# Kernel tuning notes

Measured on AMD Instinct MI355X. Metric: run time of the kernel, lower is better.

## Reference

```python
import jax, jax.numpy as jnp
import numpy as np

DIM = 2048; H = 16; DK = 128; DV = 128; SEQ = 2048; KCONV = 4
KEY_DIM = H * DK; VAL_DIM = H * DV
EPS_L2 = 1e-6; EPS_RMS = 1e-6; SP_THRESH = 20.0


def setup_inputs() -> dict:
    key = jax.random.key(0)
    ks = jax.random.split(key, 20)
    f = jnp.float32
    def w(k, shape, scale):
        return jax.random.normal(k, shape, f) * scale
    s_in = DIM ** -0.5
    return {
        "x": jax.random.normal(ks[0], (1, SEQ, DIM), f),
        "ve": jax.random.normal(ks[1], (1, SEQ, H, DV), f),
        "sa_lambdas": jnp.array([0.7, 0.3], f),
        "Wq": w(ks[2], (DIM, KEY_DIM), s_in),
        "Wk": w(ks[3], (DIM, KEY_DIM), s_in),
        "Wv": w(ks[4], (DIM, VAL_DIM), s_in),
        "conv_q": w(ks[5], (KEY_DIM, KCONV), 0.5),
        "conv_k": w(ks[6], (KEY_DIM, KCONV), 0.5),
        "conv_v": w(ks[7], (VAL_DIM, KCONV), 0.5),
        "Wf1": w(ks[8], (DIM, DV), s_in),
        "Wf2": w(ks[9], (DV, KEY_DIM), DV ** -0.5),
        "Wb": w(ks[10], (DIM, H), s_in),
        "A_log": jnp.log(jax.random.uniform(ks[11], (H,), f, 1.0, 16.0)),
        "dt_bias": jnp.zeros((KEY_DIM,), f),
        "Wg1": w(ks[12], (DIM, DV), s_in),
        "Wg2": w(ks[13], (DV, VAL_DIM), DV ** -0.5),
        "bg2": jnp.zeros((VAL_DIM,), f),
        "norm_w": jnp.ones((DV,), f),
        "Wo": w(ks[14], (VAL_DIM, DIM), VAL_DIM ** -0.5),
    }


def _short_conv_silu(u, w):
    # u: [b, s, c], w: [c, K]; causal depthwise conv + silu
    s = u.shape[1]
    up = jnp.pad(u, ((0, 0), (w.shape[1] - 1, 0), (0, 0)))
    y = sum(up[:, i:i + s, :] * w[:, i] for i in range(w.shape[1]))
    return jax.nn.silu(y)


def _l2norm(t):
    return t * jax.lax.rsqrt(jnp.sum(t * t, axis=-1, keepdims=True) + EPS_L2)


def _forward(x, ve, sa_lambdas, Wq, Wk, Wv, conv_q, conv_k, conv_v,
             Wf1, Wf2, Wb, A_log, dt_bias, Wg1, Wg2, bg2, norm_w, Wo):
    b, s, _ = x.shape  # b == 1
    q = _short_conv_silu(x @ Wq, conv_q).reshape(b, s, H, DK)
    k = _short_conv_silu(x @ Wk, conv_k).reshape(b, s, H, DK)
    v = _short_conv_silu(x @ Wv, conv_v).reshape(b, s, H, DV)
    v = sa_lambdas[0] * v + sa_lambdas[1] * ve
    # KDA gate: per-(head, key-dim) log decay
    g = ((x @ Wf1) @ Wf2).reshape(b, s, H, DK) + dt_bias.reshape(H, DK)
    sp = jnp.where(g > SP_THRESH, g, jnp.log1p(jnp.exp(jnp.minimum(g, SP_THRESH))))
    glog = -jnp.exp(A_log)[None, None, :, None] * sp  # [b,s,h,dk]
    beta = jax.nn.sigmoid(x @ Wb)  # [b,s,h]
    # l2-normalize q,k; scale q by dk^-0.5 (chunk_kda default scale)
    qn = _l2norm(q) * (DK ** -0.5)
    kn = _l2norm(k)
    # gated delta-rule recurrence over time (b==1, squeeze batch)
    def step(S, inp):
        qt, kt, vt, gt, bt = inp  # [h,dk],[h,dk],[h,dv],[h,dk],[h]
        S = S * jnp.exp(gt)[..., None]  # per-key-channel decay
        pred = jnp.einsum('hk,hkv->hv', kt, S)
        vt_new = bt[:, None] * (vt - pred)
        S = S + kt[:, :, None] * vt_new[:, None, :]
        ot = jnp.einsum('hk,hkv->hv', qt, S)
        return S, ot
    S0 = jnp.zeros((H, DK, DV), x.dtype)
    _, o = jax.lax.scan(step, S0, (qn[0], kn[0], v[0], glog[0], beta[0]))
    o = o[None]  # [1,s,h,dv]
    # sigmoid-gated RMSNorm over head_v_dim
    gate = ((x @ Wg1) @ Wg2 + bg2).reshape(b, s, H, DV)
    var = jnp.mean(o * o, axis=-1, keepdims=True)
    o = o * jax.lax.rsqrt(var + EPS_RMS) * norm_w
    o = o * jax.nn.sigmoid(gate)
    return o.reshape(b, s, VAL_DIM) @ Wo  # [1,s,dim]


def reference(x, ve, sa_lambdas, Wq, Wk, Wv, conv_q, conv_k, conv_v,
              Wf1, Wf2, Wb, A_log, dt_bias, Wg1, Wg2, bg2, norm_w, Wo):
    return _forward(x, ve, sa_lambdas, Wq, Wk, Wv, conv_q, conv_k, conv_v,
                    Wf1, Wf2, Wb, A_log, dt_bias, Wg1, Wg2, bg2, norm_w, Wo)
```

## Files before the change

### kernel.cpp

```cpp
#include <hip/hip_runtime.h>
#include <hip/hip_bf16.h>
#include <stdint.h>
#include <stddef.h>

#define SEQL 2048
#define DIMSZ 2048
#define HN 16
#define DKD 128
#define DVD 128
#define QSCALE 0.08838834764831843f

typedef __attribute__((ext_vector_type(4))) float f32x4;
typedef __attribute__((ext_vector_type(2))) float f32x2;
typedef __attribute__((ext_vector_type(8))) short bf16x8;

__device__ __forceinline__ float sigmoid_f(float x) { return 1.f / (1.f + __expf(-x)); }
__device__ __forceinline__ float bf2f(short s) {
  union { float f; unsigned int u; } t; t.u = ((unsigned int)(unsigned short)s) << 16; return t.f;
}

#define BM 128
#define BN 128
#define BKK 64

__global__ __launch_bounds__(256) void gemm_bt(
    const __hip_bfloat16* __restrict__ A, const __hip_bfloat16* __restrict__ B,
    float* __restrict__ C, int M, int N, int lda, int ldb, int klen, int accum)
{
  __shared__ __hip_bfloat16 As[BM * BKK];
  __shared__ __hip_bfloat16 Bs[BN * BKK];
  const int tid = threadIdx.x;
  const int lane = tid & 63;
  const int w = tid >> 6;
  const int wm = w >> 1, wn = w & 1;
  const int m0 = blockIdx.y * BM, n0 = blockIdx.x * BN;
  const int l15 = lane & 15, l4 = lane >> 4;
  const int kbase = blockIdx.z * klen;

  f32x4 acc[4][4] = {};

  for (int k0 = kbase; k0 < kbase + klen; k0 += BKK) {
#pragma unroll
    for (int i = 0; i < 4; ++i) {
      const int c = (w * 4 + i) * 64 + lane;
      const int row = c >> 3;
      const int colb = (c & 7) * 8;
      __builtin_amdgcn_global_load_lds(
          (const __attribute__((address_space(1))) void*)(A + (size_t)(m0 + row) * lda + k0 + colb),
          (__attribute__((address_space(3))) void*)(As + (size_t)c * 8), 16, 0, 0);
      __builtin_amdgcn_global_load_lds(
          (const __attribute__((address_space(1))) void*)(B + (size_t)(n0 + row) * ldb + k0 + colb),
          (__attribute__((address_space(3))) void*)(Bs + (size_t)c * 8), 16, 0, 0);
    }
    __syncthreads();
#pragma unroll
    for (int kk = 0; kk < BKK; kk += 32) {
      bf16x8 af[4], bfv[4];
#pragma unroll
      for (int mi = 0; mi < 4; ++mi)
        af[mi] = *(const bf16x8*)(As + (wm * 64 + mi * 16 + l15) * BKK + kk + l4 * 8);
#pragma unroll
      for (int ni = 0; ni < 4; ++ni)
        bfv[ni] = *(const bf16x8*)(Bs + (wn * 64 + ni * 16 + l15) * BKK + kk + l4 * 8);
#pragma unroll
      for (int mi = 0; mi < 4; ++mi)
#pragma unroll
        for (int ni = 0; ni < 4; ++ni)
          acc[mi][ni] = __builtin_amdgcn_mfma_f32_16x16x32_bf16(af[mi], bfv[ni], acc[mi][ni], 0, 0, 0);
    }
    __syncthreads();
  }

  float* Cz = C + (size_t)blockIdx.z * M * N;
#pragma unroll
  for (int mi = 0; mi < 4; ++mi) {
#pragma unroll
    for (int ni = 0; ni < 4; ++ni) {
      const int row = m0 + wm * 64 + mi * 16 + l4 * 4;
      const int col = n0 + wn * 64 + ni * 16 + l15;
#pragma unroll
      for (int r = 0; r < 4; ++r) {
        size_t idx = (size_t)(row + r) * N + col;
        if (accum) Cz[idx] += acc[mi][ni][r];
        else Cz[idx] = acc[mi][ni][r];
      }
    }
  }
}

__global__ __launch_bounds__(512, 1) void gemm_bt192(
    const __hip_bfloat16* __restrict__ A, const __hip_bfloat16* __restrict__ B,
    __hip_bfloat16* __restrict__ Cb, int N, int lda, int ldb, int NT)
{
  __shared__ __hip_bfloat16 lds[57344];
  const int tid = threadIdx.x;
  const int w = tid >> 6, lane = tid & 63;
  const int wm = w >> 2, wn = w & 3;
  const int l15 = lane & 15, l4 = lane >> 4;
  const int m0 = blockIdx.y * 256, n0 = blockIdx.x * 192;

  f32x4 acc[8][3] = {};
  bf16x8 a[4][2], b[2];

  auto stage_a = [&](int half, int t1) {
    const int buf = t1 & 1;
    const int k0n = ((t1 < NT) ? t1 : 0) * 64;
#pragma unroll
    for (int i = 0; i < 2; ++i) {
      const int c = i * 512 + tid;
      const int l = half * 128 + (c >> 3);
      const int kcs = (c & 7) ^ (l & 7);
      const int grow = ((l >> 6) & 1) * 128 + (l >> 7) * 64 + (l & 63);
      __builtin_amdgcn_global_load_lds(
          (const __attribute__((address_space(1))) void*)(A + (size_t)(m0 + grow) * lda + k0n + kcs * 8),
          (__attribute__((address_space(3))) void*)(lds + (size_t)buf * 28672 + half * 8192 + (size_t)c * 8),
          16, 0, 0);
    }
  };
  auto stage_b = [&](int j, int t1) {
    const int buf = t1 & 1;
    const int k0n = ((t1 < NT) ? t1 : 0) * 64;
    const int c = tid;
    const int l = j * 64 + (c >> 3);
    const int kcs = (c & 7) ^ (l & 7);
    __builtin_amdgcn_global_load_lds(
        (const __attribute__((address_space(1))) void*)(B + (size_t)(n0 + l) * ldb + k0n + kcs * 8),
        (__attribute__((address_space(3))) void*)(lds + (size_t)buf * 28672 + 16384 + j * 4096 + (size_t)c * 8),
        16, 0, 0);
  };

  auto phase = [&](size_t cb, int MQ, int NQ, bool needA) {
    if (needA) {
#pragma unroll
      for (int m2 = 0; m2 < 4; ++m2)
#pragma unroll
        for (int ks = 0; ks < 2; ++ks) {
          const int la = MQ * 128 + wm * 64 + m2 * 16 + l15;
          const int kc = ks * 4 + l4;
          a[m2][ks] = *(const bf16x8*)(lds + cb + la * 64 + (kc ^ (la & 7)) * 8);
        }
    }
#pragma unroll
    for (int ks = 0; ks < 2; ++ks) {
      const int lb = NQ * 64 + wn * 16 + l15;
      const int kc = ks * 4 + l4;
      b[ks] = *(const bf16x8*)(lds + cb + 16384 + lb * 64 + (kc ^ (lb & 7)) * 8);
    }
    __builtin_amdgcn_s_setprio(1);
#pragma unroll
    for (int m2 = 0; m2 < 4; ++m2)
#pragma unroll
      for (int ks = 0; ks < 2; ++ks)
        acc[MQ * 4 + m2][NQ] = __builtin_amdgcn_mfma_f32_16x16x32_bf16(
            a[m2][ks], b[ks], acc[MQ * 4 + m2][NQ], 0, 0, 0);
    __builtin_amdgcn_s_setprio(0);
  };

  stage_a(0, 0); stage_a(1, 0); stage_b(0, 0); stage_b(1, 0); stage_b(2, 0);

  for (int t = 0; t < NT; ++t) {
    const size_t cb = (size_t)(t & 1) * 28672;
    stage_a(0, t + 1);
    asm volatile("s_waitcnt vmcnt(4)" ::: "memory");
    __builtin_amdgcn_s_barrier();
    __builtin_amdgcn_sched_barrier(0);
    phase(cb, 0, 0, true);
    __builtin_amdgcn_s_barrier();
    stage_a(1, t + 1);
    asm volatile("s_waitcnt vmcnt(5)" ::: "memory");
    __builtin_amdgcn_s_barrier();
    __builtin_amdgcn_sched_barrier(0);
    phase(cb, 0, 1, false);
    __builtin_amdgcn_s_barrier();
    stage_b(0, t + 1);
    asm volatile("s_waitcnt vmcnt(5)" ::: "memory");
    __builtin_amdgcn_s_barrier();
    __builtin_amdgcn_sched_barrier(0);
    phase(cb, 0, 2, false);
    __builtin_amdgcn_s_barrier();
    stage_b(1, t + 1);
    __builtin_amdgcn_s_barrier();
    __builtin_amdgcn_sched_barrier(0);
    phase(cb, 1, 0, true);
    __builtin_amdgcn_s_barrier();
    stage_b(2, t + 1);
    __builtin_amdgcn_s_barrier();
    __builtin_amdgcn_sched_barrier(0);
    phase(cb, 1, 1, false);
    __builtin_amdgcn_s_barrier();
    __builtin_amdgcn_s_barrier();
    __builtin_amdgcn_sched_barrier(0);
    phase(cb, 1, 2, false);
    __builtin_amdgcn_s_barrier();
  }
  asm volatile("s_waitcnt vmcnt(0)" ::: "memory");

#pragma unroll
  for (int mi = 0; mi < 8; ++mi)
#pragma unroll
    for (int nq = 0; nq < 3; ++nq) {
      const int row = m0 + wm * 128 + mi * 16 + l4 * 4;
      const int col = n0 + nq * 64 + wn * 16 + l15;
#pragma unroll
      for (int r = 0; r < 4; ++r)
        Cb[(size_t)(row + r) * N + col] = __float2bfloat16(acc[mi][nq][r]);
    }
}

__global__ __launch_bounds__(256) void gemm_btsplit(
    const __hip_bfloat16* __restrict__ Ah, const __hip_bfloat16* __restrict__ Al,
    const __hip_bfloat16* __restrict__ Bh, const __hip_bfloat16* __restrict__ Bl,
    float* __restrict__ C, int M, int N, int lda, int ldb, int klen)
{
  __shared__ __hip_bfloat16 Ash[BM * BKK];
  __shared__ __hip_bfloat16 Asl[BM * BKK];
  __shared__ __hip_bfloat16 Bsh[BN * BKK];
  __shared__ __hip_bfloat16 Bsl[BN * BKK];
  const int tid = threadIdx.x;
  const int lane = tid & 63;
  const int w = tid >> 6;
  const int wm = w >> 1, wn = w & 1;
  const int m0 = blockIdx.y * BM, n0 = blockIdx.x * BN;
  const int l15 = lane & 15, l4 = lane >> 4;
  const int kbase = blockIdx.z * klen;

  f32x4 acc[4][4] = {};

  for (int k0 = kbase; k0 < kbase + klen; k0 += BKK) {
#pragma unroll
    for (int i = 0; i < 4; ++i) {
      const int c = (w * 4 + i) * 64 + lane;
      const int row = c >> 3;
      const int colb = (c & 7) * 8;
      const size_t go = (size_t)(m0 + row) * lda + k0 + colb;
      const size_t gn = (size_t)(n0 + row) * ldb + k0 + colb;
      __builtin_amdgcn_global_load_lds(
          (const __attribute__((address_space(1))) void*)(Ah + go),
          (__attribute__((address_space(3))) void*)(Ash + (size_t)c * 8), 16, 0, 0);
      __builtin_amdgcn_global_load_lds(
          (const __attribute__((address_space(1))) void*)(Al + go),
          (__attribute__((address_space(3))) void*)(Asl + (size_t)c * 8), 16, 0, 0);
      __builtin_amdgcn_global_load_lds(
          (const __attribute__((address_space(1))) void*)(Bh + gn),
          (__attribute__((address_space(3))) void*)(Bsh + (size_t)c * 8), 16, 0, 0);
      __builtin_amdgcn_global_load_lds(
          (const __attribute__((address_space(1))) void*)(Bl + gn),
          (__attribute__((address_space(3))) void*)(Bsl + (size_t)c * 8), 16, 0, 0);
    }
    __syncthreads();
#pragma unroll
    for (int kk = 0; kk < BKK; kk += 32) {
      bf16x8 afh[4], afl[4], bfh[4], bfl[4];
#pragma unroll
      for (int mi = 0; mi < 4; ++mi) {
        const int ao = (wm * 64 + mi * 16 + l15) * BKK + kk + l4 * 8;
        afh[mi] = *(const bf16x8*)(Ash + ao);
        afl[mi] = *(const bf16x8*)(Asl + ao);
      }
#pragma unroll
      for (int ni = 0; ni < 4; ++ni) {
        const int bo = (wn * 64 + ni * 16 + l15) * BKK + kk + l4 * 8;
        bfh[ni] = *(const bf16x8*)(Bsh + bo);
        bfl[ni] = *(const bf16x8*)(Bsl + bo);
      }
#pragma unroll
      for (int mi = 0; mi < 4; ++mi)
#pragma unroll
        for (int ni = 0; ni < 4; ++ni) {
          acc[mi][ni] = __builtin_amdgcn_mfma_f32_16x16x32_bf16(afh[mi], bfh[ni], acc[mi][ni], 0, 0, 0);
          acc[mi][ni] = __builtin_amdgcn_mfma_f32_16x16x32_bf16(afh[mi], bfl[ni], acc[mi][ni], 0, 0, 0);
          acc[mi][ni] = __builtin_amdgcn_mfma_f32_16x16x32_bf16(afl[mi], bfh[ni], acc[mi][ni], 0, 0, 0);
        }
    }
    __syncthreads();
  }

  float* Cz = C + (size_t)blockIdx.z * M * N;
#pragma unroll
  for (int mi = 0; mi < 4; ++mi) {
#pragma unroll
    for (int ni = 0; ni < 4; ++ni) {
      const int row = m0 + wm * 64 + mi * 16 + l4 * 4;
      const int col = n0 + wn * 64 + ni * 16 + l15;
#pragma unroll
      for (int r = 0; r < 4; ++r)
        Cz[(size_t)(row + r) * N + col] = acc[mi][ni][r];
    }
  }
}

__global__ __launch_bounds__(256) void prep_all_kernel(
    const float* __restrict__ x, __hip_bfloat16* __restrict__ xb, __hip_bfloat16* __restrict__ xlo,
    const float* __restrict__ Wq, const float* __restrict__ Wk,
    const float* __restrict__ Wv, const float* __restrict__ Wo,
    __hip_bfloat16* __restrict__ WqkvT, __hip_bfloat16* __restrict__ WoT,
    const float* __restrict__ Wf1, const float* __restrict__ Wg1,
    __hip_bfloat16* __restrict__ fg1h, __hip_bfloat16* __restrict__ fg1l,
    const float* __restrict__ Wf2, const float* __restrict__ Wg2,
    __hip_bfloat16* __restrict__ f2h, __hip_bfloat16* __restrict__ f2l,
    __hip_bfloat16* __restrict__ g2h)
{
  __shared__ float tile[32][33];
  const int bid = blockIdx.x;
  const int tid = threadIdx.x;
  const int tc = tid & 31, tr = tid >> 5;

  if (bid < 16384) {
    const int z = bid >> 12, rem = bid & 4095;
    const int c0 = (rem & 63) * 32, r0 = (rem >> 6) * 32;
    const float* in = (z == 0) ? Wq : (z == 1) ? Wk : (z == 2) ? Wv : Wo;
    __hip_bfloat16* outT = (z < 3) ? (WqkvT + (size_t)z * 2048 * 2048) : WoT;
#pragma unroll
    for (int i = 0; i < 4; ++i)
      tile[tr + i * 8][tc] = in[(size_t)(r0 + tr + i * 8) * 2048 + c0 + tc];
    __syncthreads();
#pragma unroll
    for (int i = 0; i < 4; ++i)
      outT[(size_t)(c0 + tr + i * 8) * 2048 + r0 + tc] = __float2bfloat16(tile[tc][tr + i * 8]);
  } else if (bid < 16896) {
    const int rem = bid - 16384;
    const int z = rem >> 8, within = rem & 255;
    const int c0 = (within & 3) * 32, r0 = (within >> 2) * 32;
    const float* in = z ? Wg1 : Wf1;
    const size_t base = (size_t)z * 128 * 2048;
#pragma unroll
    for (int i = 0; i < 4; ++i)
      tile[tr + i * 8][tc] = in[(size_t)(r0 + tr + i * 8) * 128 + c0 + tc];
    __syncthreads();
#pragma unroll
    for (int i = 0; i < 4; ++i) {
      float val = tile[tc][tr + i * 8];
      __hip_bfloat16 h = __float2bfloat16(val);
      size_t oi = base + (size_t)(c0 + tr + i * 8) * 2048 + r0 + tc;
      fg1h[oi] = h;
      fg1l[oi] = z ? __float2bfloat16(0.f) : __float2bfloat16(val - __bfloat162float(h));
    }
  } else if (bid < 17408) {
    const int rem = bid - 16896;
    const int z = rem >> 8, within = rem & 255;
    const int c0 = (within & 63) * 32, r0 = (within >> 6) * 32;
    const float* in = z ? Wg2 : Wf2;
#pragma unroll
    for (int i = 0; i < 4; ++i)
      tile[tr + i * 8][tc] = in[(size_t)(r0 + tr + i * 8) * 2048 + c0 + tc];
    __syncthreads();
#pragma unroll
    for (int i = 0; i < 4; ++i) {
      float val = tile[tc][tr + i * 8];
      __hip_bfloat16 h = __float2bfloat16(val);
      size_t oi = (size_t)(c0 + tr + i * 8) * 128 + r0 + tc;
      if (z == 0) { f2h[oi] = h; f2l[oi] = __float2bfloat16(val - __bfloat162float(h)); }
      else g2h[oi] = h;
    }
  } else {
    const int idx = (bid - 17408) * 256 + tid;
    f32x4 v = *(const f32x4*)(x + (size_t)idx * 4);
    union { __hip_bfloat16 b[4]; unsigned long long u; } ph, pl;
#pragma unroll
    for (int j = 0; j < 4; ++j) {
      float f = v[j];
      __hip_bfloat16 hh = __float2bfloat16(f);
      ph.b[j] = hh;
      pl.b[j] = __float2bfloat16(f - __bfloat162float(hh));
    }
    *(unsigned long long*)((char*)xb + (size_t)idx * 8) = ph.u;
    *(unsigned long long*)((char*)xlo + (size_t)idx * 8) = pl.u;
  }
}

__global__ __launch_bounds__(256) void reduce8_beta_kernel(
    const float* __restrict__ part, __hip_bfloat16* __restrict__ hi,
    __hip_bfloat16* __restrict__ lo, size_t chunk,
    const float* __restrict__ x, const float* __restrict__ Wb, float* __restrict__ betaT)
{
  const int tid = threadIdx.x;
  if (blockIdx.x < 512) {
    int idx = blockIdx.x * 256 + tid;
    f32x4 a = *(const f32x4*)(part + (size_t)idx * 4);
#pragma unroll
    for (int z = 1; z < 8; ++z) {
      f32x4 b = *(const f32x4*)(part + z * chunk + (size_t)idx * 4);
      a.x += b.x; a.y += b.y; a.z += b.z; a.w += b.w;
    }
    union { __hip_bfloat16 b[4]; unsigned long long u; } ph, pl;
#pragma unroll
    for (int j = 0; j < 4; ++j) {
      float f = a[j];
      __hip_bfloat16 hh = __float2bfloat16(f);
      ph.b[j] = hh;
      pl.b[j] = __float2bfloat16(f - __bfloat162float(hh));
    }
    *(unsigned long long*)((char*)hi + (size_t)idx * 8) = ph.u;
    *(unsigned long long*)((char*)lo + (size_t)idx * 8) = pl.u;
  } else {
    int idx = (blockIdx.x - 512) * 256 + tid;
    int s = idx >> 4, h = idx & 15;
    const float* xr = x + (size_t)s * DIMSZ;
    float acc = 0.f;
    for (int d = 0; d < DIMSZ; d += 4) {
      f32x4 xv = *(const f32x4*)(xr + d);
      acc = fmaf(xv.x, Wb[(size_t)(d + 0) * HN + h], acc);
      acc = fmaf(xv.y, Wb[(size_t)(d + 1) * HN + h], acc);
      acc = fmaf(xv.z, Wb[(size_t)(d + 2) * HN + h], acc);
      acc = fmaf(xv.w, Wb[(size_t)(d + 3) * HN + h], acc);
    }
    betaT[(size_t)h * SEQL + s] = 1.f / (1.f + expf(-acc));
  }
}

#define SL20(r, d) ((r) * 160 + ((d) >> 4) * 20 + ((d) & 15))

__global__ __launch_bounds__(256) void kda_pref(
    const __hip_bfloat16* __restrict__ qkv, const float* __restrict__ ve,
    const float* __restrict__ lam,
    const float* __restrict__ cwq, const float* __restrict__ cwk, const float* __restrict__ cwv,
    const float* __restrict__ gbuf,
    const float* __restrict__ dtb, const float* __restrict__ A_log,
    const float* __restrict__ betaT,
    __hip_bfloat16* __restrict__ Xgh, __hip_bfloat16* __restrict__ KTh,
    float* __restrict__ uvS, float* __restrict__ olocS, float* __restrict__ Pg)
{
  __shared__ float GL2[32 * 160];
  __shared__ float kL2[32 * 160];
  __shared__ float qL2[32 * 132];
  __shared__ float vL2[32 * 128];
  __shared__ float ALB[32][33];
  __shared__ float Bdiag[32], betaL[32];
  __shared__ float csumW[4 * 128];

  const int bid = blockIdx.x;
  const int h = bid >> 6, cc = bid & 63;
  const int tid = threadIdx.x;
  const int w = tid >> 6, lane = tid & 63;
  const size_t hc = (size_t)h * 64 + cc;
  const float Aexp = __expf(A_log[h]);

  {
    const int c = lane * 2;
    const int r0g = cc * 32 + w * 8;
    const int cg = h * 128 + c;

    f32x4 wq0 = *(const f32x4*)(cwq + (size_t)cg * 4), wq1 = *(const f32x4*)(cwq + (size_t)(cg + 1) * 4);
    f32x4 wk0 = *(const f32x4*)(cwk + (size_t)cg * 4), wk1 = *(const f32x4*)(cwk + (size_t)(cg + 1) * 4);
    f32x4 wv0 = *(const f32x4*)(cwv + (size_t)cg * 4), wv1 = *(const f32x4*)(cwv + (size_t)(cg + 1) * 4);
    f32x2 dt2 = *(const f32x2*)(dtb + cg);
    const float l0 = lam[0], l1 = lam[1];

    f32x2 xqr[11], xkr[11], xvr[11];
#pragma unroll
    for (int i = 0; i < 11; ++i) {
      const int sr = r0g - 3 + i;
      if (sr >= 0) {
        const size_t ro = (size_t)sr * 6144 + cg;
        unsigned int uq = *(const unsigned int*)(qkv + ro);
        unsigned int uk = *(const unsigned int*)(qkv + 2048 + ro);
        unsigned int uv2 = *(const unsigned int*)(qkv + 4096 + ro);
        xqr[i].x = bf2f((short)uq);   xqr[i].y = bf2f((short)(uq >> 16));
        xkr[i].x = bf2f((short)uk);   xkr[i].y = bf2f((short)(uk >> 16));
        xvr[i].x = bf2f((short)uv2);  xvr[i].y = bf2f((short)(uv2 >> 16));
      } else {
        xqr[i].x = xqr[i].y = xkr[i].x = xkr[i].y = xvr[i].x = xvr[i].y = 0.f;
      }
    }

    float gl0[8], gl1[8];
#pragma unroll
    for (int i = 0; i < 8; ++i) {
      const int rr = r0g + i;
      const int lr = w * 8 + i;
      float aq0 = 0, aq1 = 0, ak0 = 0, ak1 = 0, av0 = 0, av1 = 0;
#pragma unroll
      for (int j = 0; j < 4; ++j) {
        aq0 = fmaf(xqr[i + j].x, wq0[j], aq0); aq1 = fmaf(xqr[i + j].y, wq1[j], aq1);
        ak0 = fmaf(xkr[i + j].x, wk0[j], ak0); ak1 = fmaf(xkr[i + j].y, wk1[j], ak1);
        av0 = fmaf(xvr[i + j].x, wv0[j], av0); av1 = fmaf(xvr[i + j].y, wv1[j], av1);
      }
      float yq0 = aq0 * sigmoid_f(aq0), yq1 = aq1 * sigmoid_f(aq1);
      float yk0 = ak0 * sigmoid_f(ak0), yk1 = ak1 * sigmoid_f(ak1);
      float yv0 = av0 * sigmoid_f(av0), yv1 = av1 * sigmoid_f(av1);

      f32x2 vev = *(const f32x2*)(ve + ((size_t)rr * HN + h) * 128 + c);
      float v0 = l0 * yv0 + l1 * vev.x;
      float v1 = l0 * yv1 + l1 * vev.y;

      float ssq = yq0 * yq0 + yq1 * yq1;
      float ssk = yk0 * yk0 + yk1 * yk1;
#pragma unroll
      for (int off = 32; off > 0; off >>= 1) {
        ssq += __shfl_xor(ssq, off);
        ssk += __shfl_xor(ssk, off);
      }
      float rq = rsqrtf(ssq + 1e-6f) * QSCALE;
      float rk = rsqrtf(ssk + 1e-6f);

      f32x2 kk; kk.x = yk0 * rk; kk.y = yk1 * rk;
      f32x2 qq; qq.x = yq0 * rq; qq.y = yq1 * rq;
      f32x2 vv; vv.x = v0; vv.y = v1;
      *(f32x2*)&kL2[SL20(lr, c)] = kk;
      *(f32x2*)&qL2[lr * 132 + c] = qq;
      *(f32x2*)&vL2[lr * 128 + c] = vv;

      f32x2 gv = *(const f32x2*)(gbuf + (size_t)rr * 2048 + cg);
      float g0 = gv.x + dt2.x, g1 = gv.y + dt2.y;
      float sp0 = (g0 > 20.f) ? g0 : log1pf(__expf(fminf(g0, 20.f)));
      float sp1 = (g1 > 20.f) ? g1 : log1pf(__expf(fminf(g1, 20.f)));
      gl0[i] = -Aexp * sp0;
      gl1[i] = -Aexp * sp1;
    }
    {
      float r0 = 0.f, r1 = 0.f;
#pragma unroll
      for (int i = 0; i < 8; ++i) { r0 += gl0[i]; gl0[i] = r0; r1 += gl1[i]; gl1[i] = r1; }
      csumW[w * 128 + c] = r0;
      csumW[w * 128 + c + 1] = r1;
    }
    if (tid < 32) betaL[tid] = betaT[(size_t)h * SEQL + cc * 32 + tid];
    __syncthreads();
    {
      float p0 = 0.f, p1 = 0.f;
      for (int wp = 0; wp < w; ++wp) { p0 += csumW[wp * 128 + c]; p1 += csumW[wp * 128 + c + 1]; }
#pragma unroll
      for (int i = 0; i < 8; ++i) {
        f32x2 gg; gg.x = gl0[i] + p0; gg.y = gl1[i] + p1;
        *(f32x2*)&GL2[SL20(w * 8 + i, c)] = gg;
      }
    }
  }
  __syncthreads();

  {
    const int tg = lane >> 3, s8 = lane & 7;
    const int tt = w * 8 + tg;
    const int ds = s8 * 20;

    float Gt[16], kt[16], qt[16];
#pragma unroll
    for (int j = 0; j < 16; j += 4) {
      *(f32x4*)&Gt[j] = *(const f32x4*)&GL2[tt * 160 + ds + j];
      *(f32x4*)&kt[j] = *(const f32x4*)&kL2[tt * 160 + ds + j];
      *(f32x4*)&qt[j] = *(const f32x4*)&qL2[tt * 132 + s8 * 16 + j];
    }
    {
      float sA = 0.f, sB = 0.f;
#pragma unroll
      for (int j = 0; j < 16; ++j) { sA = fmaf(kt[j], kt[j], sA); sB = fmaf(qt[j], kt[j], sB); }
      sA += __shfl_xor(sA, 1); sA += __shfl_xor(sA, 2); sA += __shfl_xor(sA, 4);
      sB += __shfl_xor(sB, 1); sB += __shfl_xor(sB, 2); sB += __shfl_xor(sB, 4);
      if (s8 == 0) { ALB[tt][tt] = sA; Bdiag[tt] = sB; }
    }
    const int ibound = w * 8 + 7;
    for (int i = 0; i < ibound; ++i) {
      if (i < tt) {
        float sA = 0.f, sB = 0.f;
#pragma unroll
        for (int jj = 0; jj < 4; ++jj) {
          f32x4 Gi = *(const f32x4*)&GL2[i * 160 + ds + jj * 4];
          f32x4 ki = *(const f32x4*)&kL2[i * 160 + ds + jj * 4];
#pragma unroll
          for (int u = 0; u < 4; ++u) {
            float e = __expf(Gt[jj * 4 + u] - Gi[u]);
            float kid = ki[u] * e;
            sA = fmaf(kt[jj * 4 + u], kid, sA);
            sB = fmaf(qt[jj * 4 + u], kid, sB);
          }
        }
        sA += __shfl_xor(sA, 1); sA += __shfl_xor(sA, 2); sA += __shfl_xor(sA, 4);
        sB += __shfl_xor(sB, 1); sB += __shfl_xor(sB, 2); sB += __shfl_xor(sB, 4);
        if (s8 == 0) { ALB[tt][i] = sA; ALB[i][tt] = sB; }
      }
    }
  }
  __syncthreads();

  const int col = tid & 127, half = tid >> 7;
  const size_t rowbase = (size_t)(cc * 32) * 2048 + h * 128 + col;
  const int rbase = half * 16;
  {
    const float g31 = GL2[SL20(31, col)];
    size_t kb = hc * 4096 + (size_t)col * 32;
#pragma unroll
    for (int i = 0; i < 16; ++i) {
      int r = rbase + i;
      float kv = kL2[SL20(r, col)] * __expf(g31 - GL2[SL20(r, col)]);
      KTh[kb + r] = __float2bfloat16(kv);
    }
  }

  if (half == 0) {
    float expg[32];
#pragma unroll
    for (int r = 0; r < 32; ++r) expg[r] = __expf(GL2[SL20(r, col)]);

    float uvr[32], wr[32];
#pragma unroll
    for (int r = 0; r < 32; ++r) {
      float suv = 0.f, sw = 0.f;
#pragma unroll
      for (int j = 0; j < 32; ++j) {
        if (j < r) { float a = ALB[r][j]; suv = fmaf(a, uvr[j], suv); sw = fmaf(a, wr[j], sw); }
      }
      float br = betaL[r];
      float khr = kL2[SL20(r, col)] * expg[r];
      uvr[r] = br * (vL2[r * 128 + col] - suv);
      wr[r] = br * (khr - sw);
      uvS[rowbase + (size_t)r * 2048] = uvr[r];
      Xgh[hc * 8192 + (size_t)(32 + r) * 128 + col] = __float2bfloat16(wr[r]);
    }

#pragma unroll
    for (int r = 0; r < 32; ++r) {
      float qtv = qL2[r * 132 + col] * expg[r];
      float ol = 0.f;
#pragma unroll
      for (int j = 0; j < 32; ++j) {
        if (j < r) { float b = ALB[j][r]; qtv = fmaf(-b, wr[j], qtv); ol = fmaf(b, uvr[j], ol); }
      }
      { float b = Bdiag[r]; qtv = fmaf(-b, wr[r], qtv); ol = fmaf(b, uvr[r], ol); }
      Xgh[hc * 8192 + (size_t)r * 128 + col] = __float2bfloat16(qtv);
      olocS[rowbase + (size_t)r * 2048] = ol;
    }
    Pg[hc * 128 + col] = expg[31];
  }
}

#define STP 136
#define UTP 40

struct ChunkOps {
  bf16x8 ah[4];
  bf16x8 kah[2];
  f32x4 pvv[2];
  float pB[4];
};

__global__ __launch_bounds__(256) void kda_seq_gate(
    const __hip_bfloat16* __restrict__ Xgh, const __hip_bfloat16* __restrict__ KTh,
    const float* __restrict__ uvS, const float* __restrict__ olocS,
    const float* __restrict__ Pg, float* __restrict__ obuf,
    const __hip_bfloat16* __restrict__ g1b, const __hip_bfloat16* __restrict__ Wg2T,
    float* __restrict__ gatebuf)
{
  __shared__ char smem[65536];
  const int tid = threadIdx.x;
  const int w = tid >> 6, lane = tid & 63, l15 = lane & 15, l4 = lane >> 4;

  if (blockIdx.x < 128) {
    __hip_bfloat16* STh = (__hip_bfloat16*)smem;
    __hip_bfloat16* STl = STh + 16 * STP;
    __hip_bfloat16* UTh = STl + 16 * STP;
    const int h = blockIdx.x >> 3, vq = blockIdx.x & 7;
    const int v0 = vq * 16;
    const int r0 = (w & 1) * 16 + l4 * 4;
    const int isO = (w < 2);

    for (int i = tid; i < 16 * STP; i += 256) {
      STh[i] = __float2bfloat16(0.f);
      STl[i] = __float2bfloat16(0.f);
    }
    __syncthreads();

    f32x4 S[2] = {};

    auto loadops = [&](ChunkOps& o, int c) {
      const size_t hc = (size_t)h * 64 + c;
      const __hip_bfloat16* xh = Xgh + hc * 8192 + (size_t)(w * 16 + l15) * 128 + l4 * 8;
#pragma unroll
      for (int kk = 0; kk < 4; ++kk) o.ah[kk] = *(const bf16x8*)(xh + kk * 32);
      const float* pb = (isO ? olocS : uvS) + (size_t)(c * 32 + r0) * 2048 + h * 128 + v0 + l15;
#pragma unroll
      for (int r = 0; r < 4; ++r) o.pB[r] = pb[(size_t)r * 2048];
#pragma unroll
      for (int mi = 0; mi < 2; ++mi) {
        const int kd = (w * 2 + mi) * 16;
        o.kah[mi] = *(const bf16x8*)(KTh + hc * 4096 + (size_t)(kd + l15) * 32 + l4 * 8);
        o.pvv[mi] = *(const f32x4*)(Pg + hc * 128 + kd + l4 * 4);
      }
    };

    auto body = [&](ChunkOps& o, int c) {
      f32x4 Y = {};
#pragma unroll
      for (int kk = 0; kk < 4; ++kk) {
        const int so = l15 * STP + kk * 32 + l4 * 8;
        bf16x8 bh = *(const bf16x8*)(STh + so);
        bf16x8 bl = *(const bf16x8*)(STl + so);
        Y = __builtin_amdgcn_mfma_f32_16x16x32_bf16(o.ah[kk], bh, Y, 0, 0, 0);
        Y = __builtin_amdgcn_mfma_f32_16x16x32_bf16(o.ah[kk], bl, Y, 0, 0, 0);
      }

      if (isO) {
        size_t ob = (size_t)(c * 32 + r0) * 2048 + h * 128 + v0 + l15;
#pragma unroll
        for (int r = 0; r < 4; ++r)
          obuf[ob + (size_t)r * 2048] = Y[r] + o.pB[r];
      } else {
        union { __hip_bfloat16 b[4]; unsigned long long u; } uh;
#pragma unroll
        for (int r = 0; r < 4; ++r)
          uh.b[r] = __float2bfloat16(o.pB[r] - Y[r]);
        *(unsigned long long*)(UTh + l15 * UTP + r0) = uh.u;
      }
      __syncthreads();

#pragma unroll
      for (int mi = 0; mi < 2; ++mi) S[mi] *= o.pvv[mi];
      {
        bf16x8 ubh = *(const bf16x8*)(UTh + l15 * UTP + l4 * 8);
#pragma unroll
        for (int mi = 0; mi < 2; ++mi)
          S[mi] = __builtin_amdgcn_mfma_f32_16x16x32_bf16(o.kah[mi], ubh, S[mi], 0, 0, 0);
      }

#pragma unroll
      for (int mi = 0; mi < 2; ++mi) {
        const int kd0 = (w * 2 + mi) * 16 + l4 * 4;
        union { __hip_bfloat16 b[4]; unsigned long long u; } sh, sl;
#pragma unroll
        for (int r = 0; r < 4; ++r) {
          __hip_bfloat16 hh = __float2bfloat16(S[mi][r]);
          sh.b[r] = hh;
          sl.b[r] = __float2bfloat16(S[mi][r] - __bfloat162float(hh));
        }
        *(unsigned long long*)(STh + l15 * STP + kd0) = sh.u;
        *(unsigned long long*)(STl + l15 * STP + kd0) = sl.u;
      }
      __syncthreads();
    };

    ChunkOps A_, B_;
    loadops(A_, 0);
    for (int c = 0; c < 64; c += 2) {
      loadops(B_, c + 1);
      body(A_, c);
      if (c + 2 < 64) loadops(A_, c + 2);
      body(B_, c + 1);
    }
  } else {
    __hip_bfloat16* As = (__hip_bfloat16*)smem;
    __hip_bfloat16* Bs = As + BM * BKK;
    const int b2 = blockIdx.x - 128;
    const int m0 = (b2 >> 4) * BM, n0 = (b2 & 15) * BN;
    const int wm = w >> 1, wn = w & 1;

    f32x4 acc[4][4] = {};

    for (int k0 = 0; k0 < 128; k0 += BKK) {
#pragma unroll
      for (int i = 0; i < 4; ++i) {
        const int c = (w * 4 + i) * 64 + lane;
        const int row = c >> 3;
        const int colb = (c & 7) * 8;
        __builtin_amdgcn_global_load_lds(
            (const __attribute__((address_space(1))) void*)(g1b + (size_t)(m0 + row) * 256 + k0 + colb),
            (__attribute__((address_space(3))) void*)(As + (size_t)c * 8), 16, 0, 0);
        __builtin_amdgcn_global_load_lds(
            (const __attribute__((address_space(1))) void*)(Wg2T + (size_t)(n0 + row) * 128 + k0 + colb),
            (__attribute__((address_space(3))) void*)(Bs + (size_t)c * 8), 16, 0, 0);
      }
      __syncthreads();
#pragma unroll
      for (int kk = 0; kk < BKK; kk += 32) {
        bf16x8 af[4], bfv[4];
#pragma unroll
        for (int mi = 0; mi < 4; ++mi)
          af[mi] = *(const bf16x8*)(As + (wm * 64 + mi * 16 + l15) * BKK + kk + l4 * 8);
#pragma unroll
        for (int ni = 0; ni < 4; ++ni)
          bfv[ni] = *(const bf16x8*)(Bs + (wn * 64 + ni * 16 + l15) * BKK + kk + l4 * 8);
#pragma unroll
        for (int mi = 0; mi < 4; ++mi)
#pragma unroll
          for (int ni = 0; ni < 4; ++ni)
            acc[mi][ni] = __builtin_amdgcn_mfma_f32_16x16x32_bf16(af[mi], bfv[ni], acc[mi][ni], 0, 0, 0);
      }
      __syncthreads();
    }

#pragma unroll
    for (int mi = 0; mi < 4; ++mi)
#pragma unroll
      for (int ni = 0; ni < 4; ++ni) {
        const int row = m0 + wm * 64 + mi * 16 + l4 * 4;
        const int col = n0 + wn * 64 + ni * 16 + l15;
#pragma unroll
        for (int r = 0; r < 4; ++r)
          gatebuf[(size_t)(row + r) * 2048 + col] = acc[mi][ni][r];
      }
  }
}

__global__ __launch_bounds__(256) void rmsgate_kernel(
    const float* __restrict__ o, const float* __restrict__ gate,
    const float* __restrict__ bg2, const float* __restrict__ norm_w,
    __hip_bfloat16* __restrict__ og)
{
  int row = blockIdx.x * 4 + (threadIdx.x >> 6);
  int lane = threadIdx.x & 63;
  int s = row >> 4, h = row & 15;
  int j = lane * 2;
  const float* p = o + (size_t)row * 128 + j;
  f32x2 v = *(const f32x2*)p;
  float ss = v.x * v.x + v.y * v.y;
#pragma unroll
  for (int off = 32; off > 0; off >>= 1) ss += __shfl_xor(ss, off);
  float rs = rsqrtf(ss * (1.f / 128.f) + 1e-6f);
  int c = h * 128 + j;
  float g0 = gate[(size_t)s * 2048 + c] + bg2[c];
  float g1 = gate[(size_t)s * 2048 + c + 1] + bg2[c + 1];
  float o0 = v.x * rs * norm_w[j] * (1.f / (1.f + expf(-g0)));
  float o1 = v.y * rs * norm_w[j + 1] * (1.f / (1.f + expf(-g1)));
  union { __hip_bfloat16 b[2]; unsigned int u; } pk2;
  pk2.b[0] = __float2bfloat16(o0);
  pk2.b[1] = __float2bfloat16(o1);
  *(unsigned int*)((char*)og + ((size_t)s * 2048 + c) * 2) = pk2.u;
}

extern "C" void kernel_launch(void* const* d_in, const int* in_sizes, int n_in,
                              void* d_out, int out_size, void* d_ws, size_t ws_size,
                              hipStream_t stream)
{
  const float* x      = (const float*)d_in[0];
  const float* ve     = (const float*)d_in[1];
  const float* lam    = (const float*)d_in[2];
  const float* Wq     = (const float*)d_in[3];
  const float* Wk     = (const float*)d_in[4];
  const float* Wv     = (const float*)d_in[5];
  const float* cwq    = (const float*)d_in[6];
  const float* cwk    = (const float*)d_in[7];
  const float* cwv    = (const float*)d_in[8];
  const float* Wf1    = (const float*)d_in[9];
  const float* Wf2    = (const float*)d_in[10];
  const float* Wb     = (const float*)d_in[11];
  const float* A_log  = (const float*)d_in[12];
  const float* dtb    = (const float*)d_in[13];
  const float* Wg1    = (const float*)d_in[14];
  const float* Wg2    = (const float*)d_in[15];
  const float* bg2    = (const float*)d_in[16];
  const float* norm_w = (const float*)d_in[17];
  const float* Wo     = (const float*)d_in[18];
  float* out = (float*)d_out;

  const size_t S2 = (size_t)2048 * 2048;

  char* p = (char*)d_ws;
  auto alloc = [&](size_t bytes) { char* r = p; p += (bytes + 255) & ~(size_t)255; return r; };

  __hip_bfloat16* xb     = (__hip_bfloat16*)alloc(S2 * 2);
  __hip_bfloat16* WoT    = (__hip_bfloat16*)alloc(S2 * 2);
  __hip_bfloat16* Wf2hT  = (__hip_bfloat16*)alloc(2048 * 128 * 2);
  __hip_bfloat16* Wf2lT  = (__hip_bfloat16*)alloc(2048 * 128 * 2);
  __hip_bfloat16* Wg2T   = (__hip_bfloat16*)alloc(2048 * 128 * 2);
  __hip_bfloat16* Wfg1hT = (__hip_bfloat16*)alloc((size_t)256 * 2048 * 2);
  __hip_bfloat16* Wfg1lT = (__hip_bfloat16*)alloc((size_t)256 * 2048 * 2);
  __hip_bfloat16* f1g1h  = (__hip_bfloat16*)alloc((size_t)2048 * 256 * 2);
  __hip_bfloat16* f1g1l  = (__hip_bfloat16*)alloc((size_t)2048 * 256 * 2);
  float* betaT = (float*)alloc((size_t)2048 * 16 * 4);
  __hip_bfloat16* qkvb = (__hip_bfloat16*)alloc(3 * S2 * 2);
  float* gbuf  = (float*)alloc(S2 * 4);
  float* gatebuf = (float*)alloc(S2 * 4);
  float* uvS   = (float*)alloc(S2 * 4);
  float* olocS = (float*)alloc(S2 * 4);
  __hip_bfloat16* Xgh = (__hip_bfloat16*)alloc(S2 * 4);
  __hip_bfloat16* KTh = (__hip_bfloat16*)alloc(S2 * 2);
  float* Pg    = (float*)alloc((size_t)1024 * 128 * 4);

  __hip_bfloat16* WqkvT = (__hip_bfloat16*)uvS;
  __hip_bfloat16* xlo = (__hip_bfloat16*)((char*)olocS + S2 * 2);
  float* fpart = (float*)Xgh;
  float* obuf  = gbuf;
  __hip_bfloat16* og = (__hip_bfloat16*)qkvb;

  prep_all_kernel<<<21504, 256, 0, stream>>>(x, xb, xlo, Wq, Wk, Wv, Wo, WqkvT, WoT,
                                             Wf1, Wg1, Wfg1hT, Wfg1lT,
                                             Wf2, Wg2, Wf2hT, Wf2lT, Wg2T);

  gemm_bt192<<<dim3(32, 8), 512, 0, stream>>>(xb, WqkvT, qkvb, 6144, 2048, 2048, 32);

  gemm_btsplit<<<dim3(2, 16, 8), 256, 0, stream>>>(xb, xlo, Wfg1hT, Wfg1lT, fpart,
                                                   2048, 256, 2048, 2048, 256);
  reduce8_beta_kernel<<<640, 256, 0, stream>>>(fpart, f1g1h, f1g1l, (size_t)2048 * 256,
                                               x, Wb, betaT);

  gemm_btsplit<<<dim3(16, 16), 256, 0, stream>>>(f1g1h, f1g1l, Wf2hT, Wf2lT, gbuf,
                                                 2048, 2048, 256, 128, 128);

  kda_pref<<<1024, 256, 0, stream>>>(qkvb, ve, lam, cwq, cwk, cwv, gbuf, dtb, A_log, betaT,
                                     Xgh, KTh, uvS, olocS, Pg);

  kda_seq_gate<<<384, 256, 0, stream>>>(Xgh, KTh, uvS, olocS, Pg, obuf,
                                        f1g1h + 128, Wg2T, gatebuf);

  rmsgate_kernel<<<8192, 256, 0, stream>>>(obuf, gatebuf, bg2, norm_w, og);

  gemm_bt<<<dim3(16, 16), 256, 0, stream>>>(og, WoT, out, 2048, 2048, 2048, 2048, 2048, 0);
}
```

Before: 360.8 us.

## Compute off-diagonal intra-chunk KK/QK blocks with split-bf16 MFMA

The off-diagonal 8x8 and 16x16 blocks of the 32x32 intra-chunk attention matrices (k·k and q·k with decay) move from scalar per-pair dot products with shuffles to MFMA 16x16x32 bf16 tiles. Each operand is rescaled against a reference row's cumulative gate so the decay factorises. It is split into high and low bf16 parts, and three MFMAs emulate near-fp32 precision. Only the within-8-row diagonal blocks stay on the scalar path. This cuts scalar exp/FMA work and serialized inner loops, at the cost of precision risk from the reference-row exp factorisation, which can overflow or underflow for large decays.

```diff
diff --git a/kernel.cpp b/kernel.cpp
--- a/kernel.cpp
+++ b/kernel.cpp
@@ -529,44 +529,114 @@
   __syncthreads();
 
   {
-    const int tg = lane >> 3, s8 = lane & 7;
-    const int tt = w * 8 + tg;
-    const int ds = s8 * 20;
-
-    float Gt[16], kt[16], qt[16];
-#pragma unroll
-    for (int j = 0; j < 16; j += 4) {
-      *(f32x4*)&Gt[j] = *(const f32x4*)&GL2[tt * 160 + ds + j];
-      *(f32x4*)&kt[j] = *(const f32x4*)&kL2[tt * 160 + ds + j];
-      *(f32x4*)&qt[j] = *(const f32x4*)&qL2[tt * 132 + s8 * 16 + j];
-    }
+    const int m = lane & 15, quad = lane >> 4;
     {
-      float sA = 0.f, sB = 0.f;
-#pragma unroll
-      for (int j = 0; j < 16; ++j) { sA = fmaf(kt[j], kt[j], sA); sB = fmaf(qt[j], kt[j], sB); }
-      sA += __shfl_xor(sA, 1); sA += __shfl_xor(sA, 2); sA += __shfl_xor(sA, 4);
-      sB += __shfl_xor(sB, 1); sB += __shfl_xor(sB, 2); sB += __shfl_xor(sB, 4);
-      if (s8 == 0) { ALB[tt][tt] = sA; Bdiag[tt] = sB; }
-    }
-    const int ibound = w * 8 + 7;
-    for (int i = 0; i < ibound; ++i) {
-      if (i < tt) {
+      const bool useQ = (w & 1);
+      int tL, iR, ref;
+      if (w < 2)      { tL = 16 + m; iR = m;     ref = 15; }
+      else if (m < 8) { tL = 8 + m;  iR = m;     ref = 7;  }
+      else            { tL = 16 + m; iR = 8 + m; ref = 23; }
+
+      f32x4 accM = {};
+#pragma unroll
+      for (int kk = 0; kk < 4; ++kk) {
+        const int d0 = kk * 32 + quad * 8;
+        const int slb = (d0 >> 4) * 20 + (d0 & 15);
+        f32x4 gL0 = *(const f32x4*)&GL2[tL * 160 + slb];
+        f32x4 gL1 = *(const f32x4*)&GL2[tL * 160 + slb + 4];
+        f32x4 gR0 = *(const f32x4*)&GL2[iR * 160 + slb];
+        f32x4 gR1 = *(const f32x4*)&GL2[iR * 160 + slb + 4];
+        f32x4 gF0 = *(const f32x4*)&GL2[ref * 160 + slb];
+        f32x4 gF1 = *(const f32x4*)&GL2[ref * 160 + slb + 4];
+        f32x4 kR0 = *(const f32x4*)&kL2[iR * 160 + slb];
+        f32x4 kR1 = *(const f32x4*)&kL2[iR * 160 + slb + 4];
+        f32x4 vL0, vL1;
+        if (useQ) {
+          vL0 = *(const f32x4*)&qL2[tL * 132 + d0];
+          vL1 = *(const f32x4*)&qL2[tL * 132 + d0 + 4];
+        } else {
+          vL0 = *(const f32x4*)&kL2[tL * 160 + slb];
+          vL1 = *(const f32x4*)&kL2[tL * 160 + slb + 4];
+        }
+        union { bf16x8 v; unsigned short u[8]; } lh, ll, rh, rl;
+#pragma unroll
+        for (int j = 0; j < 4; ++j) {
+          float fl = vL0[j] * __expf(gL0[j] - gF0[j]);
+          float fr = kR0[j] * __expf(gF0[j] - gR0[j]);
+          __hip_bfloat16 h1 = __float2bfloat16(fl);
+          __hip_bfloat16 h1l = __float2bfloat16(fl - __bfloat162float(h1));
+          __hip_bfloat16 h2 = __float2bfloat16(fr);
+          __hip_bfloat16 h2l = __float2bfloat16(fr - __bfloat162float(h2));
+          lh.u[j] = *(const unsigned short*)&h1; ll.u[j] = *(const unsigned short*)&h1l;
+          rh.u[j] = *(const unsigned short*)&h2; rl.u[j] = *(const unsigned short*)&h2l;
+          float fl2 = vL1[j] * __expf(gL1[j] - gF1[j]);
+          float fr2 = kR1[j] * __expf(gF1[j] - gR1[j]);
+          __hip_bfloat16 h3 = __float2bfloat16(fl2);
+          __hip_bfloat16 h3l = __float2bfloat16(fl2 - __bfloat162float(h3));
+          __hip_bfloat16 h4 = __float2bfloat16(fr2);
+          __hip_bfloat16 h4l = __float2bfloat16(fr2 - __bfloat162float(h4));
+          lh.u[4 + j] = *(const unsigned short*)&h3; ll.u[4 + j] = *(const unsigned short*)&h3l;
+          rh.u[4 + j] = *(const unsigned short*)&h4; rl.u[4 + j] = *(const unsigned short*)&h4l;
+        }
+        accM = __builtin_amdgcn_mfma_f32_16x16x32_bf16(lh.v, rh.v, accM, 0, 0, 0);
+        accM = __builtin_amdgcn_mfma_f32_16x16x32_bf16(lh.v, rl.v, accM, 0, 0, 0);
+        accM = __builtin_amdgcn_mfma_f32_16x16x32_bf16(ll.v, rh.v, accM, 0, 0, 0);
+      }
+#pragma unroll
+      for (int r = 0; r < 4; ++r) {
+        const int row = quad * 4 + r;
+        const int col = m;
+        if (w < 2) {
+          if (useQ) ALB[col][16 + row] = accM[r];
+          else      ALB[16 + row][col] = accM[r];
+        } else if ((row < 8) == (col < 8)) {
+          const int t = (row < 8) ? (8 + row) : (16 + row);
+          const int i = (col < 8) ? col : (8 + col);
+          if (useQ) ALB[i][t] = accM[r];
+          else      ALB[t][i] = accM[r];
+        }
+      }
+    }
+    {
+      const int tg = lane >> 3, s8 = lane & 7;
+      const int base = w * 8;
+      const int tt = base + tg;
+      const int ds = s8 * 20;
+
+      float Gt[16], kt[16], qt[16];
+#pragma unroll
+      for (int j = 0; j < 16; j += 4) {
+        *(f32x4*)&Gt[j] = *(const f32x4*)&GL2[tt * 160 + ds + j];
+        *(f32x4*)&kt[j] = *(const f32x4*)&kL2[tt * 160 + ds + j];
+        *(f32x4*)&qt[j] = *(const f32x4*)&qL2[tt * 132 + s8 * 16 + j];
+      }
+      {
         float sA = 0.f, sB = 0.f;
 #pragma unroll
-        for (int jj = 0; jj < 4; ++jj) {
-          f32x4 Gi = *(const f32x4*)&GL2[i * 160 + ds + jj * 4];
-          f32x4 ki = *(const f32x4*)&kL2[i * 160 + ds + jj * 4];
-#pragma unroll
-          for (int u = 0; u < 4; ++u) {
-            float e = __expf(Gt[jj * 4 + u] - Gi[u]);
-            float kid = ki[u] * e;
-            sA = fmaf(kt[jj * 4 + u], kid, sA);
-            sB = fmaf(qt[jj * 4 + u], kid, sB);
-          }
-        }
+        for (int j = 0; j < 16; ++j) { sA = fmaf(kt[j], kt[j], sA); sB = fmaf(qt[j], kt[j], sB); }
         sA += __shfl_xor(sA, 1); sA += __shfl_xor(sA, 2); sA += __shfl_xor(sA, 4);
         sB += __shfl_xor(sB, 1); sB += __shfl_xor(sB, 2); sB += __shfl_xor(sB, 4);
-        if (s8 == 0) { ALB[tt][i] = sA; ALB[i][tt] = sB; }
+        if (s8 == 0) { ALB[tt][tt] = sA; Bdiag[tt] = sB; }
+      }
+      for (int i = base; i < base + 7; ++i) {
+        if (i < tt) {
+          float sA = 0.f, sB = 0.f;
+#pragma unroll
+          for (int jj = 0; jj < 4; ++jj) {
+            f32x4 Gi = *(const f32x4*)&GL2[i * 160 + ds + jj * 4];
+            f32x4 ki = *(const f32x4*)&kL2[i * 160 + ds + jj * 4];
+#pragma unroll
+            for (int u = 0; u < 4; ++u) {
+              float e = __expf(Gt[jj * 4 + u] - Gi[u]);
+              float kid = ki[u] * e;
+              sA = fmaf(kt[jj * 4 + u], kid, sA);
+              sB = fmaf(qt[jj * 4 + u], kid, sB);
+            }
+          }
+          sA += __shfl_xor(sA, 1); sA += __shfl_xor(sA, 2); sA += __shfl_xor(sA, 4);
+          sB += __shfl_xor(sB, 1); sB += __shfl_xor(sB, 2); sB += __shfl_xor(sB, 4);
+          if (s8 == 0) { ALB[tt][i] = sA; ALB[i][tt] = sB; }
+        }
       }
     }
   }
```

Measured after the change: 345.2 us. 4.3% less time.
